# Kernel optimization log

Measured on AMD Instinct MI355X. Metric: run time of the kernel, lower is better.

## Reference

```python
import jax, jax.numpy as jnp
import numpy as np


def _gcn_conv(x, edge_index, W, b):
    """PyG-style GCNConv: h = x @ W; out = D^-1/2 (A+I) D^-1/2 h + b."""
    N = x.shape[0]
    h = x @ W  # [N, F_out]
    # add self loops
    loops = jnp.arange(N, dtype=edge_index.dtype)
    src = jnp.concatenate([edge_index[0], loops])  # [E+N]
    dst = jnp.concatenate([edge_index[1], loops])  # [E+N]
    # symmetric normalization based on in-degree (incl. self loops)
    deg = jnp.zeros((N,), dtype=h.dtype).at[dst].add(1.0)
    dinv = jnp.where(deg > 0, jax.lax.rsqrt(deg), 0.0)
    norm = dinv[src] * dinv[dst]  # [E+N]
    # gather -> scale -> scatter-add
    msgs = h[src] * norm[:, None]  # [E+N, F_out]
    out = jax.ops.segment_sum(msgs, dst, num_segments=N)
    return out + b


def setup_inputs() -> dict:
    key = jax.random.key(0)
    k1, k2, k3, k4 = jax.random.split(key, 4)
    N, E, Cin, Ch, Cout = 50000, 800000, 128, 128, 64
    x = jax.random.normal(k1, (N, Cin), dtype=jnp.float32)
    edge_index = jax.random.randint(k2, (2, E), 0, N, dtype=jnp.int64)
    W1 = jax.random.normal(k3, (Cin, Ch), dtype=jnp.float32) / np.sqrt(Cin)
    b1 = jnp.zeros((Ch,), dtype=jnp.float32)
    W2 = jax.random.normal(k4, (Ch, Cout), dtype=jnp.float32) / np.sqrt(Ch)
    b2 = jnp.zeros((Cout,), dtype=jnp.float32)
    return {"x": x, "edge_index": edge_index, "W1": W1, "b1": b1, "W2": W2, "b2": b2}


def reference(x, edge_index, W1, b1, W2, b2):
    h = jax.nn.relu(_gcn_conv(x, edge_index, W1, b1))
    # F.dropout(training=self.training): eval mode -> identity
    return _gcn_conv(h, edge_index, W2, b2)
```

## Files before the change

### kernel.cpp

```cpp
#include <hip/hip_runtime.h>

typedef _Float16 f16;
typedef f16 f16x2 __attribute__((ext_vector_type(2)));
typedef f16 f16x4 __attribute__((ext_vector_type(4)));
typedef f16 f16x8 __attribute__((ext_vector_type(8)));
typedef float f32x4 __attribute__((ext_vector_type(4)));

#define BSH 7
#define BN 128
#define CHUNK 4096
#define LCAP 4096
#define NBMAX 512
#define PMAX 512

__global__ __launch_bounds__(256) void degh(const int* __restrict__ dst, int* __restrict__ histG,
                                            const float* __restrict__ W1,
                                            const float* __restrict__ W2, f16* __restrict__ w1t,
                                            f16* __restrict__ w2t, int E, int NB, int nblk) {
    const int t = threadIdx.x, blk = blockIdx.x;
    if (blk < nblk) {
        __shared__ int hist[NBMAX];
        for (int i = t; i < NB; i += 256) hist[i] = 0;
        __syncthreads();
        int lo = blk * CHUNK, hi = min(lo + CHUNK, E);
        for (int i = lo + t; i < hi; i += 256) atomicAdd(&hist[dst[i] >> BSH], 1);
        __syncthreads();
        for (int i = t; i < NB; i += 256) histG[(size_t)i * nblk + blk] = hist[i];
        return;
    }
    if (blk == nblk) {
        for (int idx = t; idx < 128 * 128; idx += 256) {
            int n = idx >> 7, k = idx & 127;
            w1t[idx] = (f16)W1[k * 128 + n];
        }
        return;
    }
    for (int idx = t; idx < 64 * 128; idx += 256) {
        int n = idx >> 7, k = idx & 127;
        w2t[idx] = (f16)W2[k * 64 + n];
    }
}

__global__ __launch_bounds__(256) void scanA(int* __restrict__ a, int* __restrict__ bsum, int L) {
    __shared__ int tmp[256];
    int tid = threadIdx.x;
    int i = blockIdx.x * 256 + tid;
    int v = (i < L) ? a[i] : 0;
    tmp[tid] = v;
    __syncthreads();
    for (int o = 1; o < 256; o <<= 1) {
        int t2 = (tid >= o) ? tmp[tid - o] : 0;
        __syncthreads();
        tmp[tid] += t2;
        __syncthreads();
    }
    if (i < L) a[i] = tmp[tid] - v;
    if (tid == 255) bsum[blockIdx.x] = tmp[255];
}

__device__ __forceinline__ void scan_partials(const int* __restrict__ bsum, int nb2,
                                              int* excl , int* work ) {
    const int t = threadIdx.x & 255;
    for (int i = t; i < PMAX; i += 256) work[i] = (i < nb2) ? bsum[i] : 0;
    __syncthreads();
    for (int o = 1; o < PMAX; o <<= 1) {
        for (int i = t; i < PMAX; i += 256) excl[i] = work[i] + ((i >= o) ? work[i - o] : 0);
        __syncthreads();
        for (int i = t; i < PMAX; i += 256) work[i] = excl[i];
        __syncthreads();
    }
    for (int i = t; i < PMAX; i += 256) excl[i] = (i == 0) ? 0 : work[i - 1];
    __syncthreads();
}

__global__ __launch_bounds__(256) void k1(const float* __restrict__ x,
                                          const f16* __restrict__ w1t,
                                          const int* __restrict__ src, const int* __restrict__ dst,
                                          const int* __restrict__ histG,
                                          const int* __restrict__ bsum, int nb2,
                                          int* __restrict__ sorted, f16* __restrict__ h, int N,
                                          int E, int NB, int nblk) {
    __shared__ union SM {
        struct {
            f16 aT[64 * 136];
            f16 bT[128 * 136];
        } g;
        struct {
            int excl[PMAX];
            int work[PMAX];
            int ofs[NBMAX];
        } p;
    } sm;
    const int t = threadIdx.x;

    if ((int)blockIdx.x < nblk) {
        const int blk = blockIdx.x;
        scan_partials(bsum, nb2, sm.p.excl, sm.p.work);
        for (int i = t; i < NB; i += 256) {
            int idx = i * nblk + blk;
            sm.p.ofs[i] = histG[idx] + sm.p.excl[idx >> 8];
        }
        __syncthreads();
        int lo = blk * CHUNK, hi = min(lo + CHUNK, E);
        for (int i = lo + t; i < hi; i += 256) {
            int d = dst[i];
            int pos = atomicAdd(&sm.p.ofs[d >> BSH], 1);
            sorted[pos] = (src[i] << BSH) | (d & (BN - 1));
        }
        return;
    }

    const int gb = blockIdx.x - nblk;
    const int row0 = gb * 64;
    {
        int r = t >> 2, s = (t & 3) * 32;
        bool ok = (row0 + r) < N;
        const float* xp = x + (size_t)(row0 + r) * 128 + s;
        f16* dp = &sm.g.aT[r * 136 + s];
#pragma unroll
        for (int c = 0; c < 4; ++c) {
            f16x8 hv;
            if (ok) {
                float4 f0 = *(const float4*)(xp + c * 8);
                float4 f1 = *(const float4*)(xp + c * 8 + 4);
                hv[0] = (f16)f0.x; hv[1] = (f16)f0.y; hv[2] = (f16)f0.z; hv[3] = (f16)f0.w;
                hv[4] = (f16)f1.x; hv[5] = (f16)f1.y; hv[6] = (f16)f1.z; hv[7] = (f16)f1.w;
            } else {
#pragma unroll
                for (int j = 0; j < 8; ++j) hv[j] = (f16)0.f;
            }
            *(f16x8*)(dp + c * 8) = hv;
        }
    }
    for (int idx = t; idx < 128 * 16; idx += 256) {
        int n = idx >> 4, c = idx & 15;
        *(f16x8*)&sm.g.bT[n * 136 + c * 8] = *(const f16x8*)&w1t[n * 128 + c * 8];
    }
    __syncthreads();

    const int w = t >> 6, lane = t & 63, m15 = lane & 15, quad = lane >> 4;
    f32x4 acc[8];
#pragma unroll
    for (int c = 0; c < 8; ++c) acc[c] = (f32x4){0.f, 0.f, 0.f, 0.f};
    const f16* ar = &sm.g.aT[(w * 16 + m15) * 136 + quad * 8];
#pragma unroll
    for (int k0 = 0; k0 < 128; k0 += 32) {
        f16x8 a = *(const f16x8*)(ar + k0);
#pragma unroll
        for (int c = 0; c < 8; ++c) {
            f16x8 b = *(const f16x8*)(&sm.g.bT[(c * 16 + m15) * 136 + k0 + quad * 8]);
            acc[c] = __builtin_amdgcn_mfma_f32_16x16x32_f16(a, b, acc[c], 0, 0, 0);
        }
    }
#pragma unroll
    for (int c = 0; c < 8; ++c)
#pragma unroll
        for (int r = 0; r < 4; ++r) {
            int row = row0 + w * 16 + quad * 4 + r;
            if (row < N) h[(size_t)row * 128 + c * 16 + m15] = (f16)acc[c][r];
        }
}

__global__ __launch_bounds__(256) void bucket_build(const int* __restrict__ histG,
                                                    const int* __restrict__ bsum, int nb2,
                                                    const int* __restrict__ sorted,
                                                    int* __restrict__ rowstart,
                                                    float* __restrict__ dinv,
                                                    int* __restrict__ csr_src, int N, int E,
                                                    int NB, int nblk) {
    __shared__ int ent[LCAP];
    __shared__ int hist[BN];
    __shared__ int lofs[BN];
    __shared__ int excl[PMAX];
    __shared__ int work[PMAX];
    const int b = blockIdx.x, t = threadIdx.x;
    scan_partials(bsum, nb2, excl, work);

    const int i0 = b * nblk;
    const int base = histG[i0] + excl[i0 >> 8];
    const int endb = (b == NB - 1) ? E : (histG[i0 + nblk] + excl[(i0 + nblk) >> 8]);
    int total = min(endb - base, LCAP);
    if (b == 0 && t == 0) rowstart[N] = E;

    for (int i = t; i < total; i += 256) ent[i] = sorted[base + i];
    if (t < BN) hist[t] = 0;
    __syncthreads();
    for (int i = t; i < total; i += 256) atomicAdd(&hist[ent[i] & (BN - 1)], 1);
    __syncthreads();
    if (t < BN) lofs[t] = hist[t];
    __syncthreads();
    for (int o = 1; o < BN; o <<= 1) {
        int v = (t < BN && t >= o) ? lofs[t - o] : 0;
        __syncthreads();
        if (t < BN) lofs[t] += v;
        __syncthreads();
    }
    if (t < BN) {
        int ex = lofs[t] - hist[t];
        int node = (b << BSH) + t;
        if (node < N) {
            rowstart[node] = base + ex;
            dinv[node] = rsqrtf((float)hist[t] + 1.0f);
        }
        lofs[t] = ex;
    }
    __syncthreads();
    for (int i = t; i < total; i += 256) {
        int e = ent[i];
        int pos = atomicAdd(&lofs[e & (BN - 1)], 1);
        csr_src[base + pos] = e >> BSH;
    }
}

__global__ __launch_bounds__(256) void gather1(const int* __restrict__ rowstart,
                                               const int* __restrict__ csr_src,
                                               const float* __restrict__ dinv,
                                               const f16* __restrict__ h,
                                               const float* __restrict__ b1,
                                               f16* __restrict__ r1, int N) {
    int wid = (blockIdx.x * 256 + threadIdx.x) >> 6;
    int lane = threadIdx.x & 63;
    int sub = lane >> 5, l32 = lane & 31;
    int node = wid * 2 + sub;
    if (node >= N) return;
    int beg = rowstart[node], end = rowstart[node + 1];
    float dn = dinv[node];
    const f16x4* hv = (const f16x4*)h;

    f16x4 sv = hv[(size_t)node * 32 + l32];
    float a0 = dn * (float)sv[0], a1 = dn * (float)sv[1];
    float a2 = dn * (float)sv[2], a3 = dn * (float)sv[3];
    int i = beg;
    for (; i + 4 <= end; i += 4) {
        int s0 = csr_src[i], s1 = csr_src[i + 1], s2 = csr_src[i + 2], s3 = csr_src[i + 3];
        float w0 = dinv[s0], w1 = dinv[s1], w2 = dinv[s2], w3 = dinv[s3];
        f16x4 v0 = hv[(size_t)s0 * 32 + l32];
        f16x4 v1 = hv[(size_t)s1 * 32 + l32];
        f16x4 v2 = hv[(size_t)s2 * 32 + l32];
        f16x4 v3 = hv[(size_t)s3 * 32 + l32];
        a0 = fmaf(w0, (float)v0[0], a0); a1 = fmaf(w0, (float)v0[1], a1);
        a2 = fmaf(w0, (float)v0[2], a2); a3 = fmaf(w0, (float)v0[3], a3);
        a0 = fmaf(w1, (float)v1[0], a0); a1 = fmaf(w1, (float)v1[1], a1);
        a2 = fmaf(w1, (float)v1[2], a2); a3 = fmaf(w1, (float)v1[3], a3);
        a0 = fmaf(w2, (float)v2[0], a0); a1 = fmaf(w2, (float)v2[1], a1);
        a2 = fmaf(w2, (float)v2[2], a2); a3 = fmaf(w2, (float)v2[3], a3);
        a0 = fmaf(w3, (float)v3[0], a0); a1 = fmaf(w3, (float)v3[1], a1);
        a2 = fmaf(w3, (float)v3[2], a2); a3 = fmaf(w3, (float)v3[3], a3);
    }
    for (; i < end; ++i) {
        int s = csr_src[i];
        float w = dinv[s];
        f16x4 v = hv[(size_t)s * 32 + l32];
        a0 = fmaf(w, (float)v[0], a0); a1 = fmaf(w, (float)v[1], a1);
        a2 = fmaf(w, (float)v[2], a2); a3 = fmaf(w, (float)v[3], a3);
    }
    float4 bb = ((const float4*)b1)[l32];
    float o0 = dn * fmaxf(fmaf(dn, a0, bb.x), 0.f);
    float o1 = dn * fmaxf(fmaf(dn, a1, bb.y), 0.f);
    float o2 = dn * fmaxf(fmaf(dn, a2, bb.z), 0.f);
    float o3 = dn * fmaxf(fmaf(dn, a3, bb.w), 0.f);
    ((f16x4*)r1)[(size_t)node * 32 + l32] = (f16x4){(f16)o0, (f16)o1, (f16)o2, (f16)o3};
}

__global__ __launch_bounds__(256) void gemm2(const f16* __restrict__ r1,
                                             const f16* __restrict__ w2t, f16* __restrict__ h2,
                                             int N) {
    __shared__ f16 aT[64 * 136];
    __shared__ f16 bT[64 * 136];
    const int t = threadIdx.x;
    const int row0 = blockIdx.x * 64;
    {
        int r = t >> 2, s = (t & 3) * 32;
        bool ok = (row0 + r) < N;
        const f16* rp = r1 + (size_t)(row0 + r) * 128 + s;
        f16* dp = &aT[r * 136 + s];
#pragma unroll
        for (int c = 0; c < 4; ++c) {
            f16x8 hv;
            if (ok) hv = *(const f16x8*)(rp + c * 8);
            else {
#pragma unroll
                for (int j = 0; j < 8; ++j) hv[j] = (f16)0.f;
            }
            *(f16x8*)(dp + c * 8) = hv;
        }
    }
    for (int idx = t; idx < 64 * 16; idx += 256) {
        int n = idx >> 4, c = idx & 15;
        *(f16x8*)&bT[n * 136 + c * 8] = *(const f16x8*)&w2t[n * 128 + c * 8];
    }
    __syncthreads();

    const int w = t >> 6, lane = t & 63, m15 = lane & 15, quad = lane >> 4;
    f32x4 acc[4];
#pragma unroll
    for (int c = 0; c < 4; ++c) acc[c] = (f32x4){0.f, 0.f, 0.f, 0.f};
    const f16* ar = &aT[(w * 16 + m15) * 136 + quad * 8];
#pragma unroll
    for (int k0 = 0; k0 < 128; k0 += 32) {
        f16x8 a = *(const f16x8*)(ar + k0);
#pragma unroll
        for (int c = 0; c < 4; ++c) {
            f16x8 b = *(const f16x8*)(&bT[(c * 16 + m15) * 136 + k0 + quad * 8]);
            acc[c] = __builtin_amdgcn_mfma_f32_16x16x32_f16(a, b, acc[c], 0, 0, 0);
        }
    }
#pragma unroll
    for (int c = 0; c < 4; ++c)
#pragma unroll
        for (int r = 0; r < 4; ++r) {
            int row = row0 + w * 16 + quad * 4 + r;
            if (row < N) h2[(size_t)row * 64 + c * 16 + m15] = (f16)acc[c][r];
        }
}

__global__ __launch_bounds__(256) void gather2(const int* __restrict__ rowstart,
                                               const int* __restrict__ csr_src,
                                               const float* __restrict__ dinv,
                                               const f16* __restrict__ h2,
                                               const float* __restrict__ b2,
                                               float* __restrict__ out, int N) {
    int wid = (blockIdx.x * 256 + threadIdx.x) >> 6;
    int lane = threadIdx.x & 63;
    int q = lane >> 4, l16 = lane & 15;
    int node = wid * 4 + q;
    if (node >= N) return;
    int beg = rowstart[node], end = rowstart[node + 1];
    float dn = dinv[node];
    const f16x4* h2v = (const f16x4*)h2;

    f16x4 sv = h2v[(size_t)node * 16 + l16];
    float a0 = (float)sv[0], a1 = (float)sv[1], a2 = (float)sv[2], a3 = (float)sv[3];
    int i = beg;
    for (; i + 4 <= end; i += 4) {
        int s0 = csr_src[i], s1 = csr_src[i + 1], s2 = csr_src[i + 2], s3 = csr_src[i + 3];
        f16x4 v0 = h2v[(size_t)s0 * 16 + l16];
        f16x4 v1 = h2v[(size_t)s1 * 16 + l16];
        f16x4 v2 = h2v[(size_t)s2 * 16 + l16];
        f16x4 v3 = h2v[(size_t)s3 * 16 + l16];
        a0 += (float)v0[0]; a1 += (float)v0[1]; a2 += (float)v0[2]; a3 += (float)v0[3];
        a0 += (float)v1[0]; a1 += (float)v1[1]; a2 += (float)v1[2]; a3 += (float)v1[3];
        a0 += (float)v2[0]; a1 += (float)v2[1]; a2 += (float)v2[2]; a3 += (float)v2[3];
        a0 += (float)v3[0]; a1 += (float)v3[1]; a2 += (float)v3[2]; a3 += (float)v3[3];
    }
    for (; i < end; ++i) {
        int s = csr_src[i];
        f16x4 v = h2v[(size_t)s * 16 + l16];
        a0 += (float)v[0]; a1 += (float)v[1]; a2 += (float)v[2]; a3 += (float)v[3];
    }
    float4 bb = ((const float4*)b2)[l16];
    float4 o;
    o.x = fmaf(dn, a0, bb.x);
    o.y = fmaf(dn, a1, bb.y);
    o.z = fmaf(dn, a2, bb.z);
    o.w = fmaf(dn, a3, bb.w);
    ((float4*)out)[(size_t)node * 16 + l16] = o;
}

extern "C" void kernel_launch(void* const* d_in, const int* in_sizes, int n_in,
                              void* d_out, int out_size, void* d_ws, size_t ws_size,
                              hipStream_t stream) {
    const float* x  = (const float*)d_in[0];
    const int*   ei = (const int*)d_in[1];
    const float* W1 = (const float*)d_in[2];
    const float* b1 = (const float*)d_in[3];
    const float* W2 = (const float*)d_in[4];
    const float* b2 = (const float*)d_in[5];

    const int N = in_sizes[0] / 128;
    const int E = in_sizes[1] / 2;
    const int* src = ei;
    const int* dst = ei + E;
    const int NB   = (N + BN - 1) >> BSH;
    const int nblk = (E + CHUNK - 1) / CHUNK;
    const int L    = NB * nblk;
    const int nb2  = (L + 255) / 256;

    char* p = (char*)d_ws;
    auto bump = [&](size_t bytes) {
        char* r = p;
        p += (bytes + 255) & ~(size_t)255;
        return r;
    };
    int*   histG    = (int*)bump((size_t)L * 4);
    int*   bsum     = (int*)bump((size_t)nb2 * 4);
    int*   sorted   = (int*)bump((size_t)E * 4);
    int*   rowstart = (int*)bump((size_t)(N + 1) * 4);
    float* dinv     = (float*)bump((size_t)N * 4);
    int*   csr_src  = (int*)bump((size_t)E * 4);
    f16*   h        = (f16*)bump((size_t)N * 128 * 2);
    f16*   r1       = (f16*)bump((size_t)N * 128 * 2);
    f16*   h2       = (f16*)bump((size_t)N * 64 * 2);
    f16*   w1t      = (f16*)bump((size_t)128 * 128 * 2);
    f16*   w2t      = (f16*)bump((size_t)64 * 128 * 2);
    float* out      = (float*)d_out;

    degh<<<nblk + 2, 256, 0, stream>>>(dst, histG, W1, W2, w1t, w2t, E, NB, nblk);
    scanA<<<nb2, 256, 0, stream>>>(histG, bsum, L);
    k1<<<nblk + (N + 63) / 64, 256, 0, stream>>>(x, w1t, src, dst, histG, bsum, nb2, sorted, h, N,
                                                 E, NB, nblk);
    bucket_build<<<NB, 256, 0, stream>>>(histG, bsum, nb2, sorted, rowstart, dinv, csr_src, N, E,
                                         NB, nblk);
    gather1<<<((N + 1) / 2 + 3) / 4, 256, 0, stream>>>(rowstart, csr_src, dinv, h, b1, r1, N);
    gemm2<<<(N + 63) / 64, 256, 0, stream>>>(r1, w2t, h2, N);
    gather2<<<((N + 3) / 4 + 3) / 4, 256, 0, stream>>>(rowstart, csr_src, dinv, h2, b2, out, N);
}
```

Before: 181.3 us.

## Restructure GCN pipeline: global degree atomics, pre-scaled h, fused gather1+gemm2

Node degrees are now computed with global atomics during the histogram pass, so dinv is ready early and the first GEMM can pre-scale h by dinv of the source row. That removes the per-edge dinv[src] lookups from the first aggregation. The partial-sum scan becomes its own single-block kernel instead of being recomputed in every block. CSR bucket building is merged with the layer-1 GEMM in one launch, and the layer-1 gather with bias and ReLU is fused into the layer-2 GEMM through shared memory, which drops the r1 intermediate. The costs are 800K global atomics, one extra memset and launch, and a fused gather+GEMM kernel that keeps only 64 rows in flight per block, which may hide gather latency less well.

After: 227.3 us. 25.4% more time.

```diff
diff --git a/kernel.cpp b/kernel.cpp
--- a/kernel.cpp
+++ b/kernel.cpp
@@ -14,7 +14,7 @@
 #define PMAX 512
 
 __global__ __launch_bounds__(256) void degh(const int* __restrict__ dst, int* __restrict__ histG,
-                                            const float* __restrict__ W1,
+                                            int* __restrict__ deg, const float* __restrict__ W1,
                                             const float* __restrict__ W2, f16* __restrict__ w1t,
                                             f16* __restrict__ w2t, int E, int NB, int nblk) {
     const int t = threadIdx.x, blk = blockIdx.x;
@@ -23,7 +23,11 @@
         for (int i = t; i < NB; i += 256) hist[i] = 0;
         __syncthreads();
         int lo = blk * CHUNK, hi = min(lo + CHUNK, E);
-        for (int i = lo + t; i < hi; i += 256) atomicAdd(&hist[dst[i] >> BSH], 1);
+        for (int i = lo + t; i < hi; i += 256) {
+            int d = dst[i];
+            atomicAdd(&hist[d >> BSH], 1);
+            atomicAdd(&deg[d], 1);
+        }
         __syncthreads();
         for (int i = t; i < NB; i += 256) histG[(size_t)i * nblk + blk] = hist[i];
         return;
@@ -41,7 +45,9 @@
     }
 }
 
-__global__ __launch_bounds__(256) void scanA(int* __restrict__ a, int* __restrict__ bsum, int L) {
+__global__ __launch_bounds__(256) void scanA(int* __restrict__ a, int* __restrict__ bsum,
+                                             const int* __restrict__ deg,
+                                             float* __restrict__ dinv, int L, int N) {
     __shared__ int tmp[256];
     int tid = threadIdx.x;
     int i = blockIdx.x * 256 + tid;
@@ -56,11 +62,13 @@
     }
     if (i < L) a[i] = tmp[tid] - v;
     if (tid == 255) bsum[blockIdx.x] = tmp[255];
-}
-
-__device__ __forceinline__ void scan_partials(const int* __restrict__ bsum, int nb2,
-                                              int* excl , int* work ) {
-    const int t = threadIdx.x & 255;
+    if (i < N) dinv[i] = rsqrtf((float)deg[i] + 1.0f);
+}
+
+__global__ __launch_bounds__(256) void scanB(int* __restrict__ bsum, int nb2) {
+    __shared__ int excl[PMAX];
+    __shared__ int work[PMAX];
+    const int t = threadIdx.x;
     for (int i = t; i < PMAX; i += 256) work[i] = (i < nb2) ? bsum[i] : 0;
     __syncthreads();
     for (int o = 1; o < PMAX; o <<= 1) {
@@ -69,48 +77,86 @@
         for (int i = t; i < PMAX; i += 256) work[i] = excl[i];
         __syncthreads();
     }
-    for (int i = t; i < PMAX; i += 256) excl[i] = (i == 0) ? 0 : work[i - 1];
-    __syncthreads();
-}
-
-__global__ __launch_bounds__(256) void k1(const float* __restrict__ x,
-                                          const f16* __restrict__ w1t,
-                                          const int* __restrict__ src, const int* __restrict__ dst,
-                                          const int* __restrict__ histG,
-                                          const int* __restrict__ bsum, int nb2,
-                                          int* __restrict__ sorted, f16* __restrict__ h, int N,
-                                          int E, int NB, int nblk) {
+    for (int i = t; i < nb2; i += 256) bsum[i] = (i == 0) ? 0 : work[i - 1];
+}
+
+__global__ __launch_bounds__(256) void placeK(const int* __restrict__ src,
+                                              const int* __restrict__ dst,
+                                              const int* __restrict__ histG,
+                                              const int* __restrict__ bsumx,
+                                              int* __restrict__ sorted, int E, int NB, int nblk) {
+    __shared__ int ofs[NBMAX];
+    const int t = threadIdx.x, blk = blockIdx.x;
+    for (int i = t; i < NB; i += 256) {
+        int idx = i * nblk + blk;
+        ofs[i] = histG[idx] + bsumx[idx >> 8];
+    }
+    __syncthreads();
+    int lo = blk * CHUNK, hi = min(lo + CHUNK, E);
+    for (int i = lo + t; i < hi; i += 256) {
+        int d = dst[i];
+        int pos = atomicAdd(&ofs[d >> BSH], 1);
+        sorted[pos] = (src[i] << BSH) | (d & (BN - 1));
+    }
+}
+
+__global__ __launch_bounds__(256) void k4(const int* __restrict__ histG,
+                                          const int* __restrict__ bsumx,
+                                          const int* __restrict__ sorted,
+                                          int* __restrict__ rowstart, int* __restrict__ csr_src,
+                                          const float* __restrict__ x, const f16* __restrict__ w1t,
+                                          const float* __restrict__ dinv, f16* __restrict__ h,
+                                          int N, int E, int NB, int nblk) {
     __shared__ union SM {
         struct {
             f16 aT[64 * 136];
             f16 bT[128 * 136];
         } g;
         struct {
-            int excl[PMAX];
-            int work[PMAX];
-            int ofs[NBMAX];
-        } p;
+            int ent[LCAP];
+            int hist[BN];
+            int lofs[BN];
+        } b;
     } sm;
     const int t = threadIdx.x;
 
-    if ((int)blockIdx.x < nblk) {
-        const int blk = blockIdx.x;
-        scan_partials(bsum, nb2, sm.p.excl, sm.p.work);
-        for (int i = t; i < NB; i += 256) {
-            int idx = i * nblk + blk;
-            sm.p.ofs[i] = histG[idx] + sm.p.excl[idx >> 8];
-        }
-        __syncthreads();
-        int lo = blk * CHUNK, hi = min(lo + CHUNK, E);
-        for (int i = lo + t; i < hi; i += 256) {
-            int d = dst[i];
-            int pos = atomicAdd(&sm.p.ofs[d >> BSH], 1);
-            sorted[pos] = (src[i] << BSH) | (d & (BN - 1));
+    if ((int)blockIdx.x < NB) {
+        const int b = blockIdx.x;
+        const int i0 = b * nblk;
+        const int base = histG[i0] + bsumx[i0 >> 8];
+        const int endb = (b == NB - 1) ? E : (histG[i0 + nblk] + bsumx[(i0 + nblk) >> 8]);
+        int total = min(endb - base, LCAP);
+        if (b == 0 && t == 0) rowstart[N] = E;
+
+        for (int i = t; i < total; i += 256) sm.b.ent[i] = sorted[base + i];
+        if (t < BN) sm.b.hist[t] = 0;
+        __syncthreads();
+        for (int i = t; i < total; i += 256) atomicAdd(&sm.b.hist[sm.b.ent[i] & (BN - 1)], 1);
+        __syncthreads();
+        if (t < BN) sm.b.lofs[t] = sm.b.hist[t];
+        __syncthreads();
+        for (int o = 1; o < BN; o <<= 1) {
+            int v = (t < BN && t >= o) ? sm.b.lofs[t - o] : 0;
+            __syncthreads();
+            if (t < BN) sm.b.lofs[t] += v;
+            __syncthreads();
+        }
+        if (t < BN) {
+            int ex = sm.b.lofs[t] - sm.b.hist[t];
+            int node = (b << BSH) + t;
+            if (node < N) rowstart[node] = base + ex;
+            sm.b.lofs[t] = ex;
+        }
+        __syncthreads();
+        for (int i = t; i < total; i += 256) {
+            int e = sm.b.ent[i];
+            int pos = atomicAdd(&sm.b.lofs[e & (BN - 1)], 1);
+            csr_src[base + pos] = e >> BSH;
         }
         return;
     }
 
-    const int gb = blockIdx.x - nblk;
+    const int gb = blockIdx.x - NB;
     const int row0 = gb * 64;
     {
         int r = t >> 2, s = (t & 3) * 32;
@@ -152,142 +198,78 @@
             acc[c] = __builtin_amdgcn_mfma_f32_16x16x32_f16(a, b, acc[c], 0, 0, 0);
         }
     }
+    const int rbase = row0 + w * 16 + quad * 4;
+    float dv[4];
+#pragma unroll
+    for (int r = 0; r < 4; ++r) {
+        int row = rbase + r;
+        dv[r] = (row < N) ? dinv[row] : 0.f;
+    }
 #pragma unroll
     for (int c = 0; c < 8; ++c)
 #pragma unroll
         for (int r = 0; r < 4; ++r) {
-            int row = row0 + w * 16 + quad * 4 + r;
-            if (row < N) h[(size_t)row * 128 + c * 16 + m15] = (f16)acc[c][r];
-        }
-}
-
-__global__ __launch_bounds__(256) void bucket_build(const int* __restrict__ histG,
-                                                    const int* __restrict__ bsum, int nb2,
-                                                    const int* __restrict__ sorted,
-                                                    int* __restrict__ rowstart,
-                                                    float* __restrict__ dinv,
-                                                    int* __restrict__ csr_src, int N, int E,
-                                                    int NB, int nblk) {
-    __shared__ int ent[LCAP];
-    __shared__ int hist[BN];
-    __shared__ int lofs[BN];
-    __shared__ int excl[PMAX];
-    __shared__ int work[PMAX];
-    const int b = blockIdx.x, t = threadIdx.x;
-    scan_partials(bsum, nb2, excl, work);
-
-    const int i0 = b * nblk;
-    const int base = histG[i0] + excl[i0 >> 8];
-    const int endb = (b == NB - 1) ? E : (histG[i0 + nblk] + excl[(i0 + nblk) >> 8]);
-    int total = min(endb - base, LCAP);
-    if (b == 0 && t == 0) rowstart[N] = E;
-
-    for (int i = t; i < total; i += 256) ent[i] = sorted[base + i];
-    if (t < BN) hist[t] = 0;
-    __syncthreads();
-    for (int i = t; i < total; i += 256) atomicAdd(&hist[ent[i] & (BN - 1)], 1);
-    __syncthreads();
-    if (t < BN) lofs[t] = hist[t];
-    __syncthreads();
-    for (int o = 1; o < BN; o <<= 1) {
-        int v = (t < BN && t >= o) ? lofs[t - o] : 0;
-        __syncthreads();
-        if (t < BN) lofs[t] += v;
-        __syncthreads();
-    }
-    if (t < BN) {
-        int ex = lofs[t] - hist[t];
-        int node = (b << BSH) + t;
-        if (node < N) {
-            rowstart[node] = base + ex;
-            dinv[node] = rsqrtf((float)hist[t] + 1.0f);
-        }
-        lofs[t] = ex;
-    }
-    __syncthreads();
-    for (int i = t; i < total; i += 256) {
-        int e = ent[i];
-        int pos = atomicAdd(&lofs[e & (BN - 1)], 1);
-        csr_src[base + pos] = e >> BSH;
-    }
-}
-
-__global__ __launch_bounds__(256) void gather1(const int* __restrict__ rowstart,
-                                               const int* __restrict__ csr_src,
-                                               const float* __restrict__ dinv,
-                                               const f16* __restrict__ h,
-                                               const float* __restrict__ b1,
-                                               f16* __restrict__ r1, int N) {
-    int wid = (blockIdx.x * 256 + threadIdx.x) >> 6;
-    int lane = threadIdx.x & 63;
-    int sub = lane >> 5, l32 = lane & 31;
-    int node = wid * 2 + sub;
-    if (node >= N) return;
-    int beg = rowstart[node], end = rowstart[node + 1];
-    float dn = dinv[node];
-    const f16x4* hv = (const f16x4*)h;
-
-    f16x4 sv = hv[(size_t)node * 32 + l32];
-    float a0 = dn * (float)sv[0], a1 = dn * (float)sv[1];
-    float a2 = dn * (float)sv[2], a3 = dn * (float)sv[3];
-    int i = beg;
-    for (; i + 4 <= end; i += 4) {
-        int s0 = csr_src[i], s1 = csr_src[i + 1], s2 = csr_src[i + 2], s3 = csr_src[i + 3];
-        float w0 = dinv[s0], w1 = dinv[s1], w2 = dinv[s2], w3 = dinv[s3];
-        f16x4 v0 = hv[(size_t)s0 * 32 + l32];
-        f16x4 v1 = hv[(size_t)s1 * 32 + l32];
-        f16x4 v2 = hv[(size_t)s2 * 32 + l32];
-        f16x4 v3 = hv[(size_t)s3 * 32 + l32];
-        a0 = fmaf(w0, (float)v0[0], a0); a1 = fmaf(w0, (float)v0[1], a1);
-        a2 = fmaf(w0, (float)v0[2], a2); a3 = fmaf(w0, (float)v0[3], a3);
-        a0 = fmaf(w1, (float)v1[0], a0); a1 = fmaf(w1, (float)v1[1], a1);
-        a2 = fmaf(w1, (float)v1[2], a2); a3 = fmaf(w1, (float)v1[3], a3);
-        a0 = fmaf(w2, (float)v2[0], a0); a1 = fmaf(w2, (float)v2[1], a1);
-        a2 = fmaf(w2, (float)v2[2], a2); a3 = fmaf(w2, (float)v2[3], a3);
-        a0 = fmaf(w3, (float)v3[0], a0); a1 = fmaf(w3, (float)v3[1], a1);
-        a2 = fmaf(w3, (float)v3[2], a2); a3 = fmaf(w3, (float)v3[3], a3);
-    }
-    for (; i < end; ++i) {
-        int s = csr_src[i];
-        float w = dinv[s];
-        f16x4 v = hv[(size_t)s * 32 + l32];
-        a0 = fmaf(w, (float)v[0], a0); a1 = fmaf(w, (float)v[1], a1);
-        a2 = fmaf(w, (float)v[2], a2); a3 = fmaf(w, (float)v[3], a3);
-    }
-    float4 bb = ((const float4*)b1)[l32];
-    float o0 = dn * fmaxf(fmaf(dn, a0, bb.x), 0.f);
-    float o1 = dn * fmaxf(fmaf(dn, a1, bb.y), 0.f);
-    float o2 = dn * fmaxf(fmaf(dn, a2, bb.z), 0.f);
-    float o3 = dn * fmaxf(fmaf(dn, a3, bb.w), 0.f);
-    ((f16x4*)r1)[(size_t)node * 32 + l32] = (f16x4){(f16)o0, (f16)o1, (f16)o2, (f16)o3};
-}
-
-__global__ __launch_bounds__(256) void gemm2(const f16* __restrict__ r1,
-                                             const f16* __restrict__ w2t, f16* __restrict__ h2,
-                                             int N) {
+            int row = rbase + r;
+            if (row < N) h[(size_t)row * 128 + c * 16 + m15] = (f16)(acc[c][r] * dv[r]);
+        }
+}
+
+__global__ __launch_bounds__(256) void fuse12(const int* __restrict__ rowstart,
+                                              const int* __restrict__ csr_src,
+                                              const float* __restrict__ dinv,
+                                              const f16* __restrict__ h,
+                                              const float* __restrict__ b1,
+                                              const f16* __restrict__ w2t,
+                                              f16* __restrict__ h2, int N) {
     __shared__ f16 aT[64 * 136];
     __shared__ f16 bT[64 * 136];
     const int t = threadIdx.x;
     const int row0 = blockIdx.x * 64;
-    {
-        int r = t >> 2, s = (t & 3) * 32;
-        bool ok = (row0 + r) < N;
-        const f16* rp = r1 + (size_t)(row0 + r) * 128 + s;
-        f16* dp = &aT[r * 136 + s];
-#pragma unroll
-        for (int c = 0; c < 4; ++c) {
-            f16x8 hv;
-            if (ok) hv = *(const f16x8*)(rp + c * 8);
-            else {
-#pragma unroll
-                for (int j = 0; j < 8; ++j) hv[j] = (f16)0.f;
-            }
-            *(f16x8*)(dp + c * 8) = hv;
-        }
-    }
+
     for (int idx = t; idx < 64 * 16; idx += 256) {
         int n = idx >> 4, c = idx & 15;
         *(f16x8*)&bT[n * 136 + c * 8] = *(const f16x8*)&w2t[n * 128 + c * 8];
+    }
+
+    const int sg = t >> 5, l32 = t & 31;
+    const float4 bb = ((const float4*)b1)[l32];
+    const f16x4* hv = (const f16x4*)h;
+
+#pragma unroll 1
+    for (int rr = 0; rr < 8; ++rr) {
+        int r = sg * 8 + rr;
+        int node = row0 + r;
+        f16x4 ov = (f16x4){(f16)0.f, (f16)0.f, (f16)0.f, (f16)0.f};
+        if (node < N) {
+            int beg = rowstart[node], end = rowstart[node + 1];
+            float dn = dinv[node];
+            f16x4 sv = hv[(size_t)node * 32 + l32];
+            float a0 = (float)sv[0], a1 = (float)sv[1], a2 = (float)sv[2], a3 = (float)sv[3];
+            int i = beg;
+            for (; i + 4 <= end; i += 4) {
+                int s0 = csr_src[i], s1 = csr_src[i + 1];
+                int s2 = csr_src[i + 2], s3 = csr_src[i + 3];
+                f16x4 v0 = hv[(size_t)s0 * 32 + l32];
+                f16x4 v1 = hv[(size_t)s1 * 32 + l32];
+                f16x4 v2 = hv[(size_t)s2 * 32 + l32];
+                f16x4 v3 = hv[(size_t)s3 * 32 + l32];
+                a0 += (float)v0[0]; a1 += (float)v0[1]; a2 += (float)v0[2]; a3 += (float)v0[3];
+                a0 += (float)v1[0]; a1 += (float)v1[1]; a2 += (float)v1[2]; a3 += (float)v1[3];
+                a0 += (float)v2[0]; a1 += (float)v2[1]; a2 += (float)v2[2]; a3 += (float)v2[3];
+                a0 += (float)v3[0]; a1 += (float)v3[1]; a2 += (float)v3[2]; a3 += (float)v3[3];
+            }
+            for (; i < end; ++i) {
+                int s = csr_src[i];
+                f16x4 v = hv[(size_t)s * 32 + l32];
+                a0 += (float)v[0]; a1 += (float)v[1]; a2 += (float)v[2]; a3 += (float)v[3];
+            }
+            float o0 = dn * fmaxf(fmaf(dn, a0, bb.x), 0.f);
+            float o1 = dn * fmaxf(fmaf(dn, a1, bb.y), 0.f);
+            float o2 = dn * fmaxf(fmaf(dn, a2, bb.z), 0.f);
+            float o3 = dn * fmaxf(fmaf(dn, a3, bb.w), 0.f);
+            ov = (f16x4){(f16)o0, (f16)o1, (f16)o2, (f16)o3};
+        }
+        *(f16x4*)&aT[r * 136 + l32 * 4] = ov;
     }
     __syncthreads();
 
@@ -384,24 +366,24 @@
     };
     int*   histG    = (int*)bump((size_t)L * 4);
     int*   bsum     = (int*)bump((size_t)nb2 * 4);
+    int*   deg      = (int*)bump((size_t)N * 4);
     int*   sorted   = (int*)bump((size_t)E * 4);
     int*   rowstart = (int*)bump((size_t)(N + 1) * 4);
     float* dinv     = (float*)bump((size_t)N * 4);
     int*   csr_src  = (int*)bump((size_t)E * 4);
     f16*   h        = (f16*)bump((size_t)N * 128 * 2);
-    f16*   r1       = (f16*)bump((size_t)N * 128 * 2);
     f16*   h2       = (f16*)bump((size_t)N * 64 * 2);
     f16*   w1t      = (f16*)bump((size_t)128 * 128 * 2);
     f16*   w2t      = (f16*)bump((size_t)64 * 128 * 2);
     float* out      = (float*)d_out;
 
-    degh<<<nblk + 2, 256, 0, stream>>>(dst, histG, W1, W2, w1t, w2t, E, NB, nblk);
-    scanA<<<nb2, 256, 0, stream>>>(histG, bsum, L);
-    k1<<<nblk + (N + 63) / 64, 256, 0, stream>>>(x, w1t, src, dst, histG, bsum, nb2, sorted, h, N,
-                                                 E, NB, nblk);
-    bucket_build<<<NB, 256, 0, stream>>>(histG, bsum, nb2, sorted, rowstart, dinv, csr_src, N, E,
-                                         NB, nblk);
-    gather1<<<((N + 1) / 2 + 3) / 4, 256, 0, stream>>>(rowstart, csr_src, dinv, h, b1, r1, N);
-    gemm2<<<(N + 63) / 64, 256, 0, stream>>>(r1, w2t, h2, N);
+    hipMemsetAsync(deg, 0, (size_t)N * 4, stream);
+    degh<<<nblk + 2, 256, 0, stream>>>(dst, histG, deg, W1, W2, w1t, w2t, E, NB, nblk);
+    scanA<<<nb2, 256, 0, stream>>>(histG, bsum, deg, dinv, L, N);
+    scanB<<<1, 256, 0, stream>>>(bsum, nb2);
+    placeK<<<nblk, 256, 0, stream>>>(src, dst, histG, bsum, sorted, E, NB, nblk);
+    k4<<<NB + (N + 63) / 64, 256, 0, stream>>>(histG, bsum, sorted, rowstart, csr_src, x, w1t,
+                                               dinv, h, N, E, NB, nblk);
+    fuse12<<<(N + 63) / 64, 256, 0, stream>>>(rowstart, csr_src, dinv, h, b1, w2t, h2, N);
     gather2<<<((N + 3) / 4 + 3) / 4, 256, 0, stream>>>(rowstart, csr_src, dinv, h2, b2, out, N);
 }
```

## Fold source-side normalization into GEMM1 epilogue and hoist partial-sum scan into own kernel

Applied to the files above, without the earlier changes.

Node degrees are now counted with global atomics in the histogram kernel, and dinv is computed in the scan kernel, so it is ready before the first GEMM. The GEMM epilogue multiplies each row of h by dinv, so the layer-1 gather no longer loads dinv per edge and does plain adds. The partial-sum scan that every sort and bucket block used to repeat is moved into a single-block scanB kernel, and its result is read directly. In exchange this adds a memset, an extra launch, and 800k global atomics on the degree array.

New measurement: 215.9 us. 19.1% more time.

```diff
diff --git a/kernel.cpp b/kernel.cpp
--- a/kernel.cpp
+++ b/kernel.cpp
@@ -14,7 +14,7 @@
 #define PMAX 512
 
 __global__ __launch_bounds__(256) void degh(const int* __restrict__ dst, int* __restrict__ histG,
-                                            const float* __restrict__ W1,
+                                            int* __restrict__ deg, const float* __restrict__ W1,
                                             const float* __restrict__ W2, f16* __restrict__ w1t,
                                             f16* __restrict__ w2t, int E, int NB, int nblk) {
     const int t = threadIdx.x, blk = blockIdx.x;
@@ -23,7 +23,11 @@
         for (int i = t; i < NB; i += 256) hist[i] = 0;
         __syncthreads();
         int lo = blk * CHUNK, hi = min(lo + CHUNK, E);
-        for (int i = lo + t; i < hi; i += 256) atomicAdd(&hist[dst[i] >> BSH], 1);
+        for (int i = lo + t; i < hi; i += 256) {
+            int d = dst[i];
+            atomicAdd(&hist[d >> BSH], 1);
+            atomicAdd(&deg[d], 1);
+        }
         __syncthreads();
         for (int i = t; i < NB; i += 256) histG[(size_t)i * nblk + blk] = hist[i];
         return;
@@ -41,7 +45,9 @@
     }
 }
 
-__global__ __launch_bounds__(256) void scanA(int* __restrict__ a, int* __restrict__ bsum, int L) {
+__global__ __launch_bounds__(256) void scanA(int* __restrict__ a, int* __restrict__ bsum,
+                                             const int* __restrict__ deg,
+                                             float* __restrict__ dinv, int L, int N) {
     __shared__ int tmp[256];
     int tid = threadIdx.x;
     int i = blockIdx.x * 256 + tid;
@@ -56,11 +62,13 @@
     }
     if (i < L) a[i] = tmp[tid] - v;
     if (tid == 255) bsum[blockIdx.x] = tmp[255];
-}
-
-__device__ __forceinline__ void scan_partials(const int* __restrict__ bsum, int nb2,
-                                              int* excl , int* work ) {
-    const int t = threadIdx.x & 255;
+    if (i < N) dinv[i] = rsqrtf((float)deg[i] + 1.0f);
+}
+
+__global__ __launch_bounds__(256) void scanB(int* __restrict__ bsum, int nb2) {
+    __shared__ int excl[PMAX];
+    __shared__ int work[PMAX];
+    const int t = threadIdx.x;
     for (int i = t; i < PMAX; i += 256) work[i] = (i < nb2) ? bsum[i] : 0;
     __syncthreads();
     for (int o = 1; o < PMAX; o <<= 1) {
@@ -69,15 +77,15 @@
         for (int i = t; i < PMAX; i += 256) work[i] = excl[i];
         __syncthreads();
     }
-    for (int i = t; i < PMAX; i += 256) excl[i] = (i == 0) ? 0 : work[i - 1];
-    __syncthreads();
+    for (int i = t; i < nb2; i += 256) bsum[i] = (i == 0) ? 0 : work[i - 1];
 }
 
 __global__ __launch_bounds__(256) void k1(const float* __restrict__ x,
                                           const f16* __restrict__ w1t,
                                           const int* __restrict__ src, const int* __restrict__ dst,
                                           const int* __restrict__ histG,
-                                          const int* __restrict__ bsum, int nb2,
+                                          const int* __restrict__ bsumx,
+                                          const float* __restrict__ dinv,
                                           int* __restrict__ sorted, f16* __restrict__ h, int N,
                                           int E, int NB, int nblk) {
     __shared__ union SM {
@@ -86,8 +94,6 @@
             f16 bT[128 * 136];
         } g;
         struct {
-            int excl[PMAX];
-            int work[PMAX];
             int ofs[NBMAX];
         } p;
     } sm;
@@ -95,10 +101,9 @@
 
     if ((int)blockIdx.x < nblk) {
         const int blk = blockIdx.x;
-        scan_partials(bsum, nb2, sm.p.excl, sm.p.work);
         for (int i = t; i < NB; i += 256) {
             int idx = i * nblk + blk;
-            sm.p.ofs[i] = histG[idx] + sm.p.excl[idx >> 8];
+            sm.p.ofs[i] = histG[idx] + bsumx[idx >> 8];
         }
         __syncthreads();
         int lo = blk * CHUNK, hi = min(lo + CHUNK, E);
@@ -152,33 +157,36 @@
             acc[c] = __builtin_amdgcn_mfma_f32_16x16x32_f16(a, b, acc[c], 0, 0, 0);
         }
     }
+    const int rbase = row0 + w * 16 + quad * 4;
+    float dv[4];
+#pragma unroll
+    for (int r = 0; r < 4; ++r) {
+        int row = rbase + r;
+        dv[r] = (row < N) ? dinv[row] : 0.f;
+    }
 #pragma unroll
     for (int c = 0; c < 8; ++c)
 #pragma unroll
         for (int r = 0; r < 4; ++r) {
-            int row = row0 + w * 16 + quad * 4 + r;
-            if (row < N) h[(size_t)row * 128 + c * 16 + m15] = (f16)acc[c][r];
+            int row = rbase + r;
+            if (row < N) h[(size_t)row * 128 + c * 16 + m15] = (f16)(acc[c][r] * dv[r]);
         }
 }
 
 __global__ __launch_bounds__(256) void bucket_build(const int* __restrict__ histG,
-                                                    const int* __restrict__ bsum, int nb2,
+                                                    const int* __restrict__ bsumx,
                                                     const int* __restrict__ sorted,
                                                     int* __restrict__ rowstart,
-                                                    float* __restrict__ dinv,
                                                     int* __restrict__ csr_src, int N, int E,
                                                     int NB, int nblk) {
     __shared__ int ent[LCAP];
     __shared__ int hist[BN];
     __shared__ int lofs[BN];
-    __shared__ int excl[PMAX];
-    __shared__ int work[PMAX];
     const int b = blockIdx.x, t = threadIdx.x;
-    scan_partials(bsum, nb2, excl, work);
 
     const int i0 = b * nblk;
-    const int base = histG[i0] + excl[i0 >> 8];
-    const int endb = (b == NB - 1) ? E : (histG[i0 + nblk] + excl[(i0 + nblk) >> 8]);
+    const int base = histG[i0] + bsumx[i0 >> 8];
+    const int endb = (b == NB - 1) ? E : (histG[i0 + nblk] + bsumx[(i0 + nblk) >> 8]);
     int total = min(endb - base, LCAP);
     if (b == 0 && t == 0) rowstart[N] = E;
 
@@ -198,10 +206,7 @@
     if (t < BN) {
         int ex = lofs[t] - hist[t];
         int node = (b << BSH) + t;
-        if (node < N) {
-            rowstart[node] = base + ex;
-            dinv[node] = rsqrtf((float)hist[t] + 1.0f);
-        }
+        if (node < N) rowstart[node] = base + ex;
         lofs[t] = ex;
     }
     __syncthreads();
@@ -228,31 +233,23 @@
     const f16x4* hv = (const f16x4*)h;
 
     f16x4 sv = hv[(size_t)node * 32 + l32];
-    float a0 = dn * (float)sv[0], a1 = dn * (float)sv[1];
-    float a2 = dn * (float)sv[2], a3 = dn * (float)sv[3];
+    float a0 = (float)sv[0], a1 = (float)sv[1], a2 = (float)sv[2], a3 = (float)sv[3];
     int i = beg;
     for (; i + 4 <= end; i += 4) {
         int s0 = csr_src[i], s1 = csr_src[i + 1], s2 = csr_src[i + 2], s3 = csr_src[i + 3];
-        float w0 = dinv[s0], w1 = dinv[s1], w2 = dinv[s2], w3 = dinv[s3];
         f16x4 v0 = hv[(size_t)s0 * 32 + l32];
         f16x4 v1 = hv[(size_t)s1 * 32 + l32];
         f16x4 v2 = hv[(size_t)s2 * 32 + l32];
         f16x4 v3 = hv[(size_t)s3 * 32 + l32];
-        a0 = fmaf(w0, (float)v0[0], a0); a1 = fmaf(w0, (float)v0[1], a1);
-        a2 = fmaf(w0, (float)v0[2], a2); a3 = fmaf(w0, (float)v0[3], a3);
-        a0 = fmaf(w1, (float)v1[0], a0); a1 = fmaf(w1, (float)v1[1], a1);
-        a2 = fmaf(w1, (float)v1[2], a2); a3 = fmaf(w1, (float)v1[3], a3);
-        a0 = fmaf(w2, (float)v2[0], a0); a1 = fmaf(w2, (float)v2[1], a1);
-        a2 = fmaf(w2, (float)v2[2], a2); a3 = fmaf(w2, (float)v2[3], a3);
-        a0 = fmaf(w3, (float)v3[0], a0); a1 = fmaf(w3, (float)v3[1], a1);
-        a2 = fmaf(w3, (float)v3[2], a2); a3 = fmaf(w3, (float)v3[3], a3);
+        a0 += (float)v0[0]; a1 += (float)v0[1]; a2 += (float)v0[2]; a3 += (float)v0[3];
+        a0 += (float)v1[0]; a1 += (float)v1[1]; a2 += (float)v1[2]; a3 += (float)v1[3];
+        a0 += (float)v2[0]; a1 += (float)v2[1]; a2 += (float)v2[2]; a3 += (float)v2[3];
+        a0 += (float)v3[0]; a1 += (float)v3[1]; a2 += (float)v3[2]; a3 += (float)v3[3];
     }
     for (; i < end; ++i) {
         int s = csr_src[i];
-        float w = dinv[s];
         f16x4 v = hv[(size_t)s * 32 + l32];
-        a0 = fmaf(w, (float)v[0], a0); a1 = fmaf(w, (float)v[1], a1);
-        a2 = fmaf(w, (float)v[2], a2); a3 = fmaf(w, (float)v[3], a3);
+        a0 += (float)v[0]; a1 += (float)v[1]; a2 += (float)v[2]; a3 += (float)v[3];
     }
     float4 bb = ((const float4*)b1)[l32];
     float o0 = dn * fmaxf(fmaf(dn, a0, bb.x), 0.f);
@@ -384,6 +381,7 @@
     };
     int*   histG    = (int*)bump((size_t)L * 4);
     int*   bsum     = (int*)bump((size_t)nb2 * 4);
+    int*   deg      = (int*)bump((size_t)N * 4);
     int*   sorted   = (int*)bump((size_t)E * 4);
     int*   rowstart = (int*)bump((size_t)(N + 1) * 4);
     float* dinv     = (float*)bump((size_t)N * 4);
@@ -395,12 +393,13 @@
     f16*   w2t      = (f16*)bump((size_t)64 * 128 * 2);
     float* out      = (float*)d_out;
 
-    degh<<<nblk + 2, 256, 0, stream>>>(dst, histG, W1, W2, w1t, w2t, E, NB, nblk);
-    scanA<<<nb2, 256, 0, stream>>>(histG, bsum, L);
-    k1<<<nblk + (N + 63) / 64, 256, 0, stream>>>(x, w1t, src, dst, histG, bsum, nb2, sorted, h, N,
-                                                 E, NB, nblk);
-    bucket_build<<<NB, 256, 0, stream>>>(histG, bsum, nb2, sorted, rowstart, dinv, csr_src, N, E,
-                                         NB, nblk);
+    hipMemsetAsync(deg, 0, (size_t)N * 4, stream);
+    degh<<<nblk + 2, 256, 0, stream>>>(dst, histG, deg, W1, W2, w1t, w2t, E, NB, nblk);
+    scanA<<<nb2, 256, 0, stream>>>(histG, bsum, deg, dinv, L, N);
+    scanB<<<1, 256, 0, stream>>>(bsum, nb2);
+    k1<<<nblk + (N + 63) / 64, 256, 0, stream>>>(x, w1t, src, dst, histG, bsum, dinv, sorted, h,
+                                                 N, E, NB, nblk);
+    bucket_build<<<NB, 256, 0, stream>>>(histG, bsum, sorted, rowstart, csr_src, N, E, NB, nblk);
     gather1<<<((N + 1) / 2 + 3) / 4, 256, 0, stream>>>(rowstart, csr_src, dinv, h, b1, r1, N);
     gemm2<<<(N + 63) / 64, 256, 0, stream>>>(r1, w2t, h2, N);
     gather2<<<((N + 3) / 4 + 3) / 4, 256, 0, stream>>>(rowstart, csr_src, dinv, h2, b2, out, N);
```
